# Kernel optimization log

Hardware: AMD Instinct MI355X
Metric: run time of the kernel (lower is better)

The kernel has to match this reference:

```python
import jax, jax.numpy as jnp
import numpy as np

N = 50000   # nodes
E = 400000  # edges
R = 35      # num_relations
B = 12      # num_bases
C = 128     # hidden_conv_dim (heads=1)
T = 4       # node types: load, gen, load_gen, ext
HL = 38     # hidden_lin_dim
OUT = 2


def setup_inputs() -> dict:
    key = jax.random.key(0)
    ks = jax.random.split(key, 24)
    s = 0.1  # param scale
    inp = {
        'x': jax.random.normal(ks[0], (N, 2), jnp.float32),
        'edge_index': jax.random.randint(ks[1], (2, E), 0, N, jnp.int32),
        'edge_type': jax.random.randint(ks[2], (E,), 0, R, jnp.int32),
        'edge_attr': jax.random.normal(ks[3], (E, 2), jnp.float32),
        'node_type': jax.random.randint(ks[4], (N,), 0, T, jnp.int32),
        'basis': jax.random.normal(ks[5], (B, 2, C), jnp.float32) * s,
        'att_rel': jax.random.normal(ks[6], (R, B), jnp.float32) * s,
        'q_att': jax.random.normal(ks[7], (C, 1), jnp.float32) * s,
        'k_att': jax.random.normal(ks[8], (C, 1), jnp.float32) * s,
        'e_att': jax.random.normal(ks[9], (C, 1), jnp.float32) * s,
        'lin_edge_W': jax.random.normal(ks[10], (2, C), jnp.float32) * s,
        'conv_bias': jax.random.normal(ks[11], (C,), jnp.float32) * s,
        'lin0_W': jax.random.normal(ks[12], (T, C, HL), jnp.float32) * s,
        'lin0_b': jax.random.normal(ks[13], (T, HL), jnp.float32) * s,
        'lin1_W': jax.random.normal(ks[14], (T, HL, HL), jnp.float32) * s,
        'lin1_b': jax.random.normal(ks[15], (T, HL), jnp.float32) * s,
        'lin2_W': jax.random.normal(ks[16], (T, HL, HL), jnp.float32) * s,
        'lin2_b': jax.random.normal(ks[17], (T, HL), jnp.float32) * s,
        'fin_W': jax.random.normal(ks[18], (T, HL, OUT), jnp.float32) * s,
        'fin_b': jax.random.normal(ks[19], (T, OUT), jnp.float32) * s,
    }
    return inp


def _segment_softmax(alpha, dst, n):
    # PyG softmax: max is detached, eps=1e-16 on the denominator
    amax = jax.lax.stop_gradient(jax.ops.segment_max(alpha, dst, num_segments=n))
    ex = jnp.exp(alpha - amax[dst])
    den = jax.ops.segment_sum(ex, dst, num_segments=n) + 1e-16
    return ex / den[dst]


def _per_type_linear(xv, W, b, t):
    # apply node-type-specific Linear: [N,d] x [T,d,h] -> pick row type
    y = jnp.einsum('nd,tdh->nth', xv, W)              # [N,T,h]
    y = jnp.take_along_axis(y, t[:, None, None], axis=1)[:, 0]
    return y + b[t]


def reference(x, edge_index, edge_type, edge_attr, node_type,
              basis, att_rel, q_att, k_att, e_att, lin_edge_W, conv_bias,
              lin0_W, lin0_b, lin1_W, lin1_b, lin2_W, lin2_b, fin_W, fin_b):
    n = x.shape[0]
    src, dst = edge_index[0], edge_index[1]
    # RGATConv with basis decomposition: per-relation weight [R, in=2, C]
    w = jnp.einsum('rb,bio->rio', att_rel, basis)
    w_e = w[edge_type]                                 # [E,2,C] edge gather
    out_i = jnp.einsum('ei,eic->ec', x[dst], w_e)      # [E,C]
    out_j = jnp.einsum('ei,eic->ec', x[src], w_e)      # [E,C]
    ke = (edge_attr @ lin_edge_W) @ e_att              # [E,1]
    alpha = out_i @ q_att + out_j @ k_att + ke         # additive self-attention
    alpha = jax.nn.leaky_relu(alpha, 0.2)
    alpha = _segment_softmax(alpha, dst, n)            # across-relation segment softmax
    msg = alpha * out_j                                # heads=1 -> [E,C]
    agg = jax.ops.segment_sum(msg, dst, num_segments=n) + conv_bias
    h = jax.nn.leaky_relu(agg, 0.2)                    # forward activation (dropout: eval)
    t = node_type
    h = _per_type_linear(jax.nn.relu(h), lin0_W, lin0_b, t)
    h = _per_type_linear(jax.nn.relu(h), lin1_W, lin1_b, t)
    h = _per_type_linear(jax.nn.relu(h), lin2_W, lin2_b, t)
    out = _per_type_linear(h, fin_W, fin_b, t)         # [N,2]
    # load nodes (type 0): second output passes through abs
    load_out = jnp.concatenate([out[:, :1], jnp.abs(out[:, 1:2])], axis=1)
    return jnp.where((t == 0)[:, None], load_out, out)
```

## Files before the change

kernel.cpp:

```cpp
#include <hip/hip_runtime.h>
#include <math.h>

#define N_NODES 50000
#define N_EDGES 400000
#define R_REL   35
#define B_BASES 12
#define C_DIM   128
#define HL_DIM  38
#define RI2     70
#define NP      50304
#define NB_HIST 196
#define NBUCK   786
#define EPB     2048
#define CAP     704

#define OFF_WT     0
#define OFF_WQ     8960
#define OFF_WK     9030
#define OFF_LE     9100
#define OFF_META   9104
#define OFF_HBLK   9120
#define OFF_PERM   10688
#define OFF_INV    60688
#define OFF_ECUR   110992
#define OFF_EREC   111780
#define OFF_W0P    2325156
#define OFF_W1P    2345636
#define OFF_W2P    2351716

#define ST    0
#define HH    0
#define Y0T   0
#define Y1T   3264
#define Y2T   0
#define SM_DINV 8192
#define SM_FW   8256
#define SM_FB   8332
#define LDS_FLOATS 8334

__global__ __launch_bounds__(256) void k_init(const int* __restrict__ node_type,
                                              const float* __restrict__ basis,
                                              const float* __restrict__ att_rel,
                                              const float* __restrict__ q_att,
                                              const float* __restrict__ k_att,
                                              const float* __restrict__ e_att,
                                              const float* __restrict__ lin_edge_W,
                                              const float* __restrict__ lin0_W,
                                              const float* __restrict__ lin1_W,
                                              const float* __restrict__ lin2_W,
                                              float* __restrict__ ws) {
    int b = blockIdx.x, tid = threadIdx.x;
    if (b < NB_HIST) {
        __shared__ int lh[4];
        if (tid < 4) lh[tid] = 0;
        __syncthreads();
        int i = b * 256 + tid;
        if (i < N_NODES) atomicAdd(&lh[node_type[i]], 1);
        __syncthreads();
        if (tid < 4) ((int*)(ws + OFF_HBLK))[b * 4 + tid] = lh[tid];
    } else if (b < NB_HIST + 35) {
        int idx = (b - NB_HIST) * 256 + tid;
        if (idx < RI2 * C_DIM) {
            int c  = idx & (C_DIM - 1);
            int ri = idx >> 7;
            int r = ri >> 1, ii = ri & 1;
            float acc = 0.f;
            #pragma unroll
            for (int bb = 0; bb < B_BASES; ++bb)
                acc += att_rel[r * B_BASES + bb] * basis[(bb * 2 + ii) * C_DIM + c];
            ws[OFF_WT + idx] = acc;
        }
    } else if (b == NB_HIST + 35) {
        for (int i = tid; i < NBUCK; i += 256) ((int*)(ws + OFF_ECUR))[i] = 0;
    } else if (b < NB_HIST + 36 + 36) {
        int lane = tid & 63, wv = tid >> 6;
        int u = (b - (NB_HIST + 36)) * 4 + wv;
        if (u < 2 * RI2) {
            int ri = (u < RI2) ? u : (u - RI2);
            int r = ri >> 1, ii = ri & 1;
            const float* av = att_rel + r * B_BASES;
            const float* bs = basis + ii * C_DIM;
            float w1 = 0.f, w2 = 0.f;
            #pragma unroll
            for (int bb = 0; bb < B_BASES; ++bb) {
                float a = av[bb];
                w1 += a * bs[bb * 2 * C_DIM + lane];
                w2 += a * bs[bb * 2 * C_DIM + 64 + lane];
            }
            const float* qk = (u < RI2) ? q_att : k_att;
            float s = w1 * qk[lane] + w2 * qk[64 + lane];
            #pragma unroll
            for (int off = 32; off; off >>= 1) s += __shfl_xor(s, off, 64);
            if (lane == 0) ws[((u < RI2) ? OFF_WQ : OFF_WK) + ri] = s;
        } else if (u < 2 * RI2 + 2) {
            int j = u - 2 * RI2;
            const float* er = lin_edge_W + j * C_DIM;
            float s = er[lane] * e_att[lane] + er[64 + lane] * e_att[64 + lane];
            #pragma unroll
            for (int off = 32; off; off >>= 1) s += __shfl_xor(s, off, 64);
            if (lane == 0) ws[OFF_LE + j] = s;
        }
    } else {
        int g = (b - (NB_HIST + 36 + 36)) * 256 + tid;
        for (int idx = g; idx < 4 * C_DIM * HL_DIM; idx += 16 * 256) {
            int tt = idx / (C_DIM * HL_DIM);
            int rem = idx - tt * (C_DIM * HL_DIM);
            int cc = rem / HL_DIM, j = rem - cc * HL_DIM;
            ws[OFF_W0P + tt * (C_DIM * 40) + cc * 40 + j] = lin0_W[idx];
        }
        for (int idx = g; idx < 4 * HL_DIM * HL_DIM; idx += 16 * 256) {
            int tt = idx / (HL_DIM * HL_DIM);
            int rem = idx - tt * (HL_DIM * HL_DIM);
            int cc = rem / HL_DIM, j = rem - cc * HL_DIM;
            ws[OFF_W1P + tt * (HL_DIM * 40) + cc * 40 + j] = lin1_W[idx];
            ws[OFF_W2P + tt * (HL_DIM * 40) + cc * 40 + j] = lin2_W[idx];
        }
    }
}

__global__ __launch_bounds__(256) void k_perm(const int* __restrict__ node_type,
                                              float* __restrict__ ws) {
    __shared__ int lh[NB_HIST * 4];
    __shared__ int pre[4], tot[4], basel[4];
    __shared__ int wcnt[4][4];
    int tid = threadIdx.x;
    int lane = tid & 63, wv = tid >> 6;
    const int* hblk = (const int*)(ws + OFF_HBLK);
    for (int i = tid; i < NB_HIST * 4; i += 256) lh[i] = hblk[i];
    __syncthreads();
    if (tid < 4) {
        int run = 0, mypre = 0;
        for (int bb = 0; bb < NB_HIST; ++bb) {
            if (bb == (int)blockIdx.x) mypre = run;
            run += lh[bb * 4 + tid];
        }
        pre[tid] = mypre;
        tot[tid] = run;
    }
    __syncthreads();
    if (tid == 0) {
        int t0 = tot[0], t1 = tot[1], t2 = tot[2];
        int b1 = ((t0 + 63) >> 6) << 6;
        int b2 = b1 + (((t1 + 63) >> 6) << 6);
        int b3 = b2 + (((t2 + 63) >> 6) << 6);
        basel[0] = 0; basel[1] = b1; basel[2] = b2; basel[3] = b3;
        if (blockIdx.x == 0) {
            int* meta = (int*)(ws + OFF_META);
            meta[0] = t0; meta[1] = t1; meta[2] = t2; meta[3] = tot[3];
            meta[4] = 0;  meta[5] = b1; meta[6] = b2; meta[7] = b3;
        }
    }
    __syncthreads();
    int n = blockIdx.x * 256 + tid;
    bool active = n < N_NODES;
    int ty = active ? node_type[n] : -1;
    int myrank = 0;
    #pragma unroll
    for (int t = 0; t < 4; ++t) {
        unsigned long long m = __ballot(ty == t);
        if (lane == 0) wcnt[wv][t] = __popcll(m);
        if (ty == t) myrank = __popcll(m & ((1ULL << lane) - 1ULL));
    }
    __syncthreads();
    if (active) {
        int prew = 0;
        for (int w2 = 0; w2 < wv; ++w2) prew += wcnt[w2][ty];
        int p = basel[ty] + pre[ty] + prew + myrank;
        ((int*)(ws + OFF_PERM))[n] = p;
        ((int*)(ws + OFF_INV))[p] = n;
    }
}

__global__ __launch_bounds__(256) void k_escatter(const float* __restrict__ x,
                                                  const int* __restrict__ edge_index,
                                                  const int* __restrict__ edge_type,
                                                  const float* __restrict__ edge_attr,
                                                  float* __restrict__ ws) {
    __shared__ int hist[NBUCK];
    __shared__ int sbase[NBUCK];
    __shared__ float swq[RI2], swk[RI2], sle[2];
    int tid = threadIdx.x;
    for (int i = tid; i < NBUCK; i += 256) hist[i] = 0;
    if (tid < RI2) { swq[tid] = ws[OFF_WQ + tid]; swk[tid] = ws[OFF_WK + tid]; }
    if (tid < 2) sle[tid] = ws[OFF_LE + tid];
    __syncthreads();

    const int* perm = (const int*)(ws + OFF_PERM);
    int base = blockIdx.x * EPB;
    int   rb[8], rm[8];
    float rex[8], rsx[8], rsy[8];
    #pragma unroll
    for (int k = 0; k < 8; ++k) {
        int e = base + k * 256 + tid;
        rb[k] = -1;
        if (e < N_EDGES) {
            int src = edge_index[e];
            int dst = edge_index[N_EDGES + e];
            int r   = edge_type[e];
            int p   = perm[dst];
            float2 ea = *(const float2*)(edge_attr + 2 * e);
            float2 xs = *(const float2*)(x + 2 * src);
            float2 xd = *(const float2*)(x + 2 * dst);
            float alpha = xd.x * swq[2 * r] + xd.y * swq[2 * r + 1]
                        + xs.x * swk[2 * r] + xs.y * swk[2 * r + 1]
                        + ea.x * sle[0]     + ea.y * sle[1];
            alpha = alpha > 0.f ? alpha : 0.2f * alpha;
            float ex = __expf(alpha);
            rb[k]  = p >> 6;
            rm[k]  = (r << 6) | (p & 63);
            rex[k] = ex;
            rsx[k] = ex * xs.x;
            rsy[k] = ex * xs.y;
            atomicAdd(&hist[rb[k]], 1);
        }
    }
    __syncthreads();
    int* gcur = (int*)(ws + OFF_ECUR);
    for (int i = tid; i < NBUCK; i += 256) {
        int c = hist[i];
        sbase[i] = (c > 0) ? atomicAdd(&gcur[i], c) : 0;
    }
    __syncthreads();
    float4* rec = (float4*)(ws + OFF_EREC);
    #pragma unroll
    for (int k = 0; k < 8; ++k) {
        if (rb[k] >= 0) {
            int slot = atomicAdd(&sbase[rb[k]], 1);
            rec[(size_t)rb[k] * CAP + slot] =
                make_float4(__int_as_float(rm[k]), rex[k], rsx[k], rsy[k]);
        }
    }
}

__global__ __launch_bounds__(256, 4) void k_node(
        const float* __restrict__ ws, const float* __restrict__ conv_bias,
        const float* __restrict__ lin0_b, const float* __restrict__ lin1_b,
        const float* __restrict__ lin2_b, const float* __restrict__ fin_W,
        const float* __restrict__ fin_b, float* __restrict__ out) {
    __shared__ float L[LDS_FLOATS];
    int tid  = threadIdx.x;
    int lane = tid & 63;
    int wv   = tid >> 6;
    int p0   = blockIdx.x * 64;

    const int* meta = (const int*)(ws + OFF_META);
    int b1 = meta[5], b2 = meta[6], b3 = meta[7];
    int t  = (p0 >= b1) + (p0 >= b2) + (p0 >= b3);
    int bp = meta[4 + t];
    int cnt = meta[t];

    for (int i4 = tid; i4 < (RI2 * 68) / 4; i4 += 256)
        *(float4*)&L[ST + i4 * 4] = make_float4(0.f, 0.f, 0.f, 0.f);
    if (tid < 64) L[SM_DINV + tid] = 0.f;
    if (tid >= 64 && tid < 142) {
        int i = tid - 64;
        if (i < 76) L[SM_FW + i] = fin_W[t * 76 + i];
        else        L[SM_FB + i - 76] = fin_b[t * 2 + i - 76];
    }
    __syncthreads();

    {
        int ecnt = ((const int*)(ws + OFF_ECUR))[blockIdx.x];
        const float4* rec = (const float4*)(ws + OFF_EREC) + (size_t)blockIdx.x * CAP;
        for (int i = tid; i < ecnt; i += 256) {
            float4 v = rec[i];
            int m = __float_as_int(v.x);
            int n = m & 63, r = m >> 6;
            atomicAdd(&L[ST + (2 * r) * 68 + n],     v.z);
            atomicAdd(&L[ST + (2 * r + 1) * 68 + n], v.w);
            atomicAdd(&L[SM_DINV + n],               v.y);
        }
    }
    __syncthreads();
    if (tid < 64) L[SM_DINV + tid] = 1.0f / (L[SM_DINV + tid] + 1e-16f);

    int ng = lane & 15, cg_ = lane >> 4;
    int c0 = wv * 32 + cg_ * 8;
    const float* wTg = ws + OFF_WT;
    float acc[32];
    #pragma unroll
    for (int i = 0; i < 32; ++i) acc[i] = 0.f;
    #pragma unroll 5
    for (int kk = 0; kk < RI2; ++kk) {
        float4 a4 = *(const float4*)&L[ST + kk * 68 + ng * 4];
        float4 wa = *(const float4*)&wTg[kk * 128 + c0];
        float4 wc = *(const float4*)&wTg[kk * 128 + c0 + 4];
        float a_[4] = {a4.x, a4.y, a4.z, a4.w};
        float w_[8] = {wa.x, wa.y, wa.z, wa.w, wc.x, wc.y, wc.z, wc.w};
        #pragma unroll
        for (int ni = 0; ni < 4; ++ni)
            #pragma unroll
            for (int ci = 0; ci < 8; ++ci)
                acc[ni * 8 + ci] += a_[ni] * w_[ci];
    }
    __syncthreads();

    {
        float4 dv = *(const float4*)&L[SM_DINV + ng * 4];
        float d_[4] = {dv.x, dv.y, dv.z, dv.w};
        #pragma unroll
        for (int ci = 0; ci < 8; ++ci) {
            float cb = conv_bias[c0 + ci];
            float4 hv;
            float h0 = acc[0 * 8 + ci] * d_[0] + cb;
            float h1 = acc[1 * 8 + ci] * d_[1] + cb;
            float h2 = acc[2 * 8 + ci] * d_[2] + cb;
            float h3 = acc[3 * 8 + ci] * d_[3] + cb;
            hv.x = h0 > 0.f ? h0 : 0.f;
            hv.y = h1 > 0.f ? h1 : 0.f;
            hv.z = h2 > 0.f ? h2 : 0.f;
            hv.w = h3 > 0.f ? h3 : 0.f;
            *(float4*)&L[HH + (c0 + ci) * 64 + ng * 4] = hv;
        }
    }
    __syncthreads();

    int jg = lane >> 4;
    int j0 = wv * 16 + jg * 4;
    const float* W0g = ws + OFF_W0P + t * (C_DIM * 40);
    float acc2[16];
    #pragma unroll
    for (int i = 0; i < 16; ++i) acc2[i] = 0.f;
    if (wv < 3) {
        #pragma unroll 4
        for (int kk = 0; kk < C_DIM; ++kk) {
            float4 a4 = *(const float4*)&L[HH + kk * 64 + ng * 4];
            float4 w4 = *(const float4*)&W0g[kk * 40 + j0];
            float a_[4] = {a4.x, a4.y, a4.z, a4.w};
            float w_[4] = {w4.x, w4.y, w4.z, w4.w};
            #pragma unroll
            for (int ni = 0; ni < 4; ++ni)
                #pragma unroll
                for (int ji = 0; ji < 4; ++ji)
                    acc2[ni * 4 + ji] += a_[ni] * w_[ji];
        }
    }
    __syncthreads();

    if (wv < 3) {
        #pragma unroll
        for (int ji = 0; ji < 4; ++ji) {
            int j = j0 + ji;
            float b = (j < HL_DIM) ? lin0_b[t * HL_DIM + j] : 0.f;
            float4 yv;
            float y0 = acc2[0 * 4 + ji] + b;
            float y1 = acc2[1 * 4 + ji] + b;
            float y2 = acc2[2 * 4 + ji] + b;
            float y3 = acc2[3 * 4 + ji] + b;
            yv.x = y0 > 0.f ? y0 : 0.f;
            yv.y = y1 > 0.f ? y1 : 0.f;
            yv.z = y2 > 0.f ? y2 : 0.f;
            yv.w = y3 > 0.f ? y3 : 0.f;
            *(float4*)&L[Y0T + j * 68 + ng * 4] = yv;
        }
    }
    __syncthreads();

    if (wv < 3) {
        const float* W1g = ws + OFF_W1P + t * (HL_DIM * 40);
        float acc3[16];
        #pragma unroll
        for (int i = 0; i < 16; ++i) acc3[i] = 0.f;
        #pragma unroll 2
        for (int kk = 0; kk < HL_DIM; ++kk) {
            float4 a4 = *(const float4*)&L[Y0T + kk * 68 + ng * 4];
            float4 w4 = *(const float4*)&W1g[kk * 40 + j0];
            float a_[4] = {a4.x, a4.y, a4.z, a4.w};
            float w_[4] = {w4.x, w4.y, w4.z, w4.w};
            #pragma unroll
            for (int ni = 0; ni < 4; ++ni)
                #pragma unroll
                for (int ji = 0; ji < 4; ++ji)
                    acc3[ni * 4 + ji] += a_[ni] * w_[ji];
        }
        #pragma unroll
        for (int ji = 0; ji < 4; ++ji) {
            int j = j0 + ji;
            float b = (j < HL_DIM) ? lin1_b[t * HL_DIM + j] : 0.f;
            float4 yv;
            float y0 = acc3[0 * 4 + ji] + b;
            float y1 = acc3[1 * 4 + ji] + b;
            float y2 = acc3[2 * 4 + ji] + b;
            float y3 = acc3[3 * 4 + ji] + b;
            yv.x = y0 > 0.f ? y0 : 0.f;
            yv.y = y1 > 0.f ? y1 : 0.f;
            yv.z = y2 > 0.f ? y2 : 0.f;
            yv.w = y3 > 0.f ? y3 : 0.f;
            *(float4*)&L[Y1T + j * 68 + ng * 4] = yv;
        }
    }
    __syncthreads();

    if (wv < 3) {
        const float* W2g = ws + OFF_W2P + t * (HL_DIM * 40);
        float acc4[16];
        #pragma unroll
        for (int i = 0; i < 16; ++i) acc4[i] = 0.f;
        #pragma unroll 2
        for (int kk = 0; kk < HL_DIM; ++kk) {
            float4 a4 = *(const float4*)&L[Y1T + kk * 68 + ng * 4];
            float4 w4 = *(const float4*)&W2g[kk * 40 + j0];
            float a_[4] = {a4.x, a4.y, a4.z, a4.w};
            float w_[4] = {w4.x, w4.y, w4.z, w4.w};
            #pragma unroll
            for (int ni = 0; ni < 4; ++ni)
                #pragma unroll
                for (int ji = 0; ji < 4; ++ji)
                    acc4[ni * 4 + ji] += a_[ni] * w_[ji];
        }
        #pragma unroll
        for (int ji = 0; ji < 4; ++ji) {
            int j = j0 + ji;
            float b = (j < HL_DIM) ? lin2_b[t * HL_DIM + j] : 0.f;
            float4 yv;
            yv.x = acc4[0 * 4 + ji] + b;
            yv.y = acc4[1 * 4 + ji] + b;
            yv.z = acc4[2 * 4 + ji] + b;
            yv.w = acc4[3 * 4 + ji] + b;
            *(float4*)&L[Y2T + j * 68 + ng * 4] = yv;
        }
    }
    __syncthreads();

    if (tid < 64) {
        int p = p0 + tid;
        bool valid = (p - bp) < cnt;
        float o0 = L[SM_FB], o1 = L[SM_FB + 1];
        for (int jj = 0; jj < HL_DIM; ++jj) {
            float v = L[Y2T + jj * 68 + tid];
            float2 f = *(const float2*)&L[SM_FW + jj * 2];
            o0 += v * f.x;
            o1 += v * f.y;
        }
        if (t == 0) o1 = fabsf(o1);
        if (valid) {
            int orig = ((const int*)(ws + OFF_INV))[p];
            ((float2*)out)[orig] = make_float2(o0, o1);
        }
    }
}

extern "C" void kernel_launch(void* const* d_in, const int* in_sizes, int n_in,
                              void* d_out, int out_size, void* d_ws, size_t ws_size,
                              hipStream_t stream) {
    const float* x          = (const float*)d_in[0];
    const int*   edge_index = (const int*)  d_in[1];
    const int*   edge_type  = (const int*)  d_in[2];
    const float* edge_attr  = (const float*)d_in[3];
    const int*   node_type  = (const int*)  d_in[4];
    const float* basis      = (const float*)d_in[5];
    const float* att_rel    = (const float*)d_in[6];
    const float* q_att      = (const float*)d_in[7];
    const float* k_att      = (const float*)d_in[8];
    const float* e_att      = (const float*)d_in[9];
    const float* lin_edge_W = (const float*)d_in[10];
    const float* conv_bias  = (const float*)d_in[11];
    const float* lin0_W     = (const float*)d_in[12];
    const float* lin0_b     = (const float*)d_in[13];
    const float* lin1_W     = (const float*)d_in[14];
    const float* lin1_b     = (const float*)d_in[15];
    const float* lin2_W     = (const float*)d_in[16];
    const float* lin2_b     = (const float*)d_in[17];
    const float* fin_W      = (const float*)d_in[18];
    const float* fin_b      = (const float*)d_in[19];

    float* ws  = (float*)d_ws;
    float* out = (float*)d_out;

    k_init    <<<NB_HIST + 35 + 1 + 36 + 16, 256, 0, stream>>>(node_type, basis, att_rel,
                                                               q_att, k_att, e_att, lin_edge_W,
                                                               lin0_W, lin1_W, lin2_W, ws);
    k_perm    <<<NB_HIST, 256, 0, stream>>>(node_type, ws);
    k_escatter<<<NB_HIST, 256, 0, stream>>>(x, edge_index, edge_type, edge_attr, ws);
    k_node    <<<NBUCK, 256, 0, stream>>>(ws, conv_bias,
                                          lin0_b, lin1_b, lin2_b, fin_W, fin_b, out);
}
```

Baseline: 168.6 us.

## Merge init and perm kernels; fold weight prep into edge scatter

Cuts the launch chain from four kernels to three. The type histogram and block prefix are now computed redundantly in every block of the new k_prep kernel, which rescans all node types, instead of a separate histogram pass. The basis-combine and weight-packing work moves into extra blocks of k_escatter. The q/k attention scalars are recomputed per block via an algebraic refactoring: basis·q dot products first, then combined with att_rel. The cost is that each of the 196 blocks rereads the 50000 node types, plus some redundant per-block prep.

Result: slower. 203.0 us (+20.4%).

```diff
diff --git a/kernel.cpp b/kernel.cpp
--- a/kernel.cpp
+++ b/kernel.cpp
@@ -15,11 +15,7 @@
 #define CAP     704
 
 #define OFF_WT     0
-#define OFF_WQ     8960
-#define OFF_WK     9030
-#define OFF_LE     9100
 #define OFF_META   9104
-#define OFF_HBLK   9120
 #define OFF_PERM   10688
 #define OFF_INV    60688
 #define OFF_ECUR   110992
@@ -38,120 +34,56 @@
 #define SM_FB   8332
 #define LDS_FLOATS 8334
 
-__global__ __launch_bounds__(256) void k_init(const int* __restrict__ node_type,
-                                              const float* __restrict__ basis,
-                                              const float* __restrict__ att_rel,
-                                              const float* __restrict__ q_att,
-                                              const float* __restrict__ k_att,
-                                              const float* __restrict__ e_att,
-                                              const float* __restrict__ lin_edge_W,
-                                              const float* __restrict__ lin0_W,
-                                              const float* __restrict__ lin1_W,
-                                              const float* __restrict__ lin2_W,
+__global__ __launch_bounds__(256) void k_prep(const int* __restrict__ node_type,
                                               float* __restrict__ ws) {
     int b = blockIdx.x, tid = threadIdx.x;
-    if (b < NB_HIST) {
-        __shared__ int lh[4];
-        if (tid < 4) lh[tid] = 0;
-        __syncthreads();
-        int i = b * 256 + tid;
-        if (i < N_NODES) atomicAdd(&lh[node_type[i]], 1);
-        __syncthreads();
-        if (tid < 4) ((int*)(ws + OFF_HBLK))[b * 4 + tid] = lh[tid];
-    } else if (b < NB_HIST + 35) {
-        int idx = (b - NB_HIST) * 256 + tid;
-        if (idx < RI2 * C_DIM) {
-            int c  = idx & (C_DIM - 1);
-            int ri = idx >> 7;
-            int r = ri >> 1, ii = ri & 1;
-            float acc = 0.f;
-            #pragma unroll
-            for (int bb = 0; bb < B_BASES; ++bb)
-                acc += att_rel[r * B_BASES + bb] * basis[(bb * 2 + ii) * C_DIM + c];
-            ws[OFF_WT + idx] = acc;
-        }
-    } else if (b == NB_HIST + 35) {
+    if (b >= NB_HIST) {
         for (int i = tid; i < NBUCK; i += 256) ((int*)(ws + OFF_ECUR))[i] = 0;
-    } else if (b < NB_HIST + 36 + 36) {
-        int lane = tid & 63, wv = tid >> 6;
-        int u = (b - (NB_HIST + 36)) * 4 + wv;
-        if (u < 2 * RI2) {
-            int ri = (u < RI2) ? u : (u - RI2);
-            int r = ri >> 1, ii = ri & 1;
-            const float* av = att_rel + r * B_BASES;
-            const float* bs = basis + ii * C_DIM;
-            float w1 = 0.f, w2 = 0.f;
-            #pragma unroll
-            for (int bb = 0; bb < B_BASES; ++bb) {
-                float a = av[bb];
-                w1 += a * bs[bb * 2 * C_DIM + lane];
-                w2 += a * bs[bb * 2 * C_DIM + 64 + lane];
-            }
-            const float* qk = (u < RI2) ? q_att : k_att;
-            float s = w1 * qk[lane] + w2 * qk[64 + lane];
-            #pragma unroll
-            for (int off = 32; off; off >>= 1) s += __shfl_xor(s, off, 64);
-            if (lane == 0) ws[((u < RI2) ? OFF_WQ : OFF_WK) + ri] = s;
-        } else if (u < 2 * RI2 + 2) {
-            int j = u - 2 * RI2;
-            const float* er = lin_edge_W + j * C_DIM;
-            float s = er[lane] * e_att[lane] + er[64 + lane] * e_att[64 + lane];
-            #pragma unroll
-            for (int off = 32; off; off >>= 1) s += __shfl_xor(s, off, 64);
-            if (lane == 0) ws[OFF_LE + j] = s;
-        }
-    } else {
-        int g = (b - (NB_HIST + 36 + 36)) * 256 + tid;
-        for (int idx = g; idx < 4 * C_DIM * HL_DIM; idx += 16 * 256) {
-            int tt = idx / (C_DIM * HL_DIM);
-            int rem = idx - tt * (C_DIM * HL_DIM);
-            int cc = rem / HL_DIM, j = rem - cc * HL_DIM;
-            ws[OFF_W0P + tt * (C_DIM * 40) + cc * 40 + j] = lin0_W[idx];
-        }
-        for (int idx = g; idx < 4 * HL_DIM * HL_DIM; idx += 16 * 256) {
-            int tt = idx / (HL_DIM * HL_DIM);
-            int rem = idx - tt * (HL_DIM * HL_DIM);
-            int cc = rem / HL_DIM, j = rem - cc * HL_DIM;
-            ws[OFF_W1P + tt * (HL_DIM * 40) + cc * 40 + j] = lin1_W[idx];
-            ws[OFF_W2P + tt * (HL_DIM * 40) + cc * 40 + j] = lin2_W[idx];
-        }
-    }
-}
-
-__global__ __launch_bounds__(256) void k_perm(const int* __restrict__ node_type,
-                                              float* __restrict__ ws) {
-    __shared__ int lh[NB_HIST * 4];
-    __shared__ int pre[4], tot[4], basel[4];
+        return;
+    }
+    __shared__ int sred[4][8];
+    __shared__ int fin[8];
+    __shared__ int basel[4];
     __shared__ int wcnt[4][4];
-    int tid = threadIdx.x;
     int lane = tid & 63, wv = tid >> 6;
-    const int* hblk = (const int*)(ws + OFF_HBLK);
-    for (int i = tid; i < NB_HIST * 4; i += 256) lh[i] = hblk[i];
-    __syncthreads();
-    if (tid < 4) {
-        int run = 0, mypre = 0;
-        for (int bb = 0; bb < NB_HIST; ++bb) {
-            if (bb == (int)blockIdx.x) mypre = run;
-            run += lh[bb * 4 + tid];
-        }
-        pre[tid] = mypre;
-        tot[tid] = run;
-    }
+    int limit = b * 256;
+
+    int n0 = 0, n1 = 0, n2 = 0, n3 = 0, q0 = 0, q1 = 0, q2 = 0, q3 = 0;
+    for (int i = tid; i < N_NODES; i += 256) {
+        int ty = node_type[i];
+        int lt = (i < limit) ? 1 : 0;
+        n0 += (ty == 0); n1 += (ty == 1); n2 += (ty == 2); n3 += (ty == 3);
+        q0 += (ty == 0) & lt; q1 += (ty == 1) & lt;
+        q2 += (ty == 2) & lt; q3 += (ty == 3) & lt;
+    }
+    #pragma unroll
+    for (int off = 32; off; off >>= 1) {
+        n0 += __shfl_xor(n0, off, 64); n1 += __shfl_xor(n1, off, 64);
+        n2 += __shfl_xor(n2, off, 64); n3 += __shfl_xor(n3, off, 64);
+        q0 += __shfl_xor(q0, off, 64); q1 += __shfl_xor(q1, off, 64);
+        q2 += __shfl_xor(q2, off, 64); q3 += __shfl_xor(q3, off, 64);
+    }
+    if (lane == 0) {
+        sred[wv][0] = n0; sred[wv][1] = n1; sred[wv][2] = n2; sred[wv][3] = n3;
+        sred[wv][4] = q0; sred[wv][5] = q1; sred[wv][6] = q2; sred[wv][7] = q3;
+    }
+    __syncthreads();
+    if (tid < 8) fin[tid] = sred[0][tid] + sred[1][tid] + sred[2][tid] + sred[3][tid];
     __syncthreads();
     if (tid == 0) {
-        int t0 = tot[0], t1 = tot[1], t2 = tot[2];
+        int t0 = fin[0], t1 = fin[1], t2 = fin[2];
         int b1 = ((t0 + 63) >> 6) << 6;
         int b2 = b1 + (((t1 + 63) >> 6) << 6);
         int b3 = b2 + (((t2 + 63) >> 6) << 6);
         basel[0] = 0; basel[1] = b1; basel[2] = b2; basel[3] = b3;
-        if (blockIdx.x == 0) {
+        if (b == 0) {
             int* meta = (int*)(ws + OFF_META);
-            meta[0] = t0; meta[1] = t1; meta[2] = t2; meta[3] = tot[3];
+            meta[0] = t0; meta[1] = t1; meta[2] = t2; meta[3] = fin[3];
             meta[4] = 0;  meta[5] = b1; meta[6] = b2; meta[7] = b3;
         }
     }
     __syncthreads();
-    int n = blockIdx.x * 256 + tid;
+    int n = b * 256 + tid;
     bool active = n < N_NODES;
     int ty = active ? node_type[n] : -1;
     int myrank = 0;
@@ -165,7 +97,7 @@
     if (active) {
         int prew = 0;
         for (int w2 = 0; w2 < wv; ++w2) prew += wcnt[w2][ty];
-        int p = basel[ty] + pre[ty] + prew + myrank;
+        int p = basel[ty] + fin[4 + ty] + prew + myrank;
         ((int*)(ws + OFF_PERM))[n] = p;
         ((int*)(ws + OFF_INV))[p] = n;
     }
@@ -175,18 +107,87 @@
                                                   const int* __restrict__ edge_index,
                                                   const int* __restrict__ edge_type,
                                                   const float* __restrict__ edge_attr,
+                                                  const float* __restrict__ basis,
+                                                  const float* __restrict__ att_rel,
+                                                  const float* __restrict__ q_att,
+                                                  const float* __restrict__ k_att,
+                                                  const float* __restrict__ e_att,
+                                                  const float* __restrict__ lin_edge_W,
+                                                  const float* __restrict__ lin0_W,
+                                                  const float* __restrict__ lin1_W,
+                                                  const float* __restrict__ lin2_W,
                                                   float* __restrict__ ws) {
+    int b = blockIdx.x, tid = threadIdx.x;
+    if (b >= NB_HIST) {
+        if (b < NB_HIST + 35) {
+            int idx = (b - NB_HIST) * 256 + tid;
+            if (idx < RI2 * C_DIM) {
+                int c  = idx & (C_DIM - 1);
+                int ri = idx >> 7;
+                int r = ri >> 1, ii = ri & 1;
+                float acc = 0.f;
+                #pragma unroll
+                for (int bb = 0; bb < B_BASES; ++bb)
+                    acc += att_rel[r * B_BASES + bb] * basis[(bb * 2 + ii) * C_DIM + c];
+                ws[OFF_WT + idx] = acc;
+            }
+        } else {
+            int g = (b - (NB_HIST + 35)) * 256 + tid;
+            for (int idx = g; idx < 4 * C_DIM * HL_DIM; idx += 16 * 256) {
+                int tt = idx / (C_DIM * HL_DIM);
+                int rem = idx - tt * (C_DIM * HL_DIM);
+                int cc = rem / HL_DIM, j = rem - cc * HL_DIM;
+                ws[OFF_W0P + tt * (C_DIM * 40) + cc * 40 + j] = lin0_W[idx];
+            }
+            for (int idx = g; idx < 4 * HL_DIM * HL_DIM; idx += 16 * 256) {
+                int tt = idx / (HL_DIM * HL_DIM);
+                int rem = idx - tt * (HL_DIM * HL_DIM);
+                int cc = rem / HL_DIM, j = rem - cc * HL_DIM;
+                ws[OFF_W1P + tt * (HL_DIM * 40) + cc * 40 + j] = lin1_W[idx];
+                ws[OFF_W2P + tt * (HL_DIM * 40) + cc * 40 + j] = lin2_W[idx];
+            }
+        }
+        return;
+    }
+
     __shared__ int hist[NBUCK];
     __shared__ int sbase[NBUCK];
     __shared__ float swq[RI2], swk[RI2], sle[2];
-    int tid = threadIdx.x;
+    __shared__ float s_dot[64];
+    int lane = tid & 63, wv = tid >> 6;
+
     for (int i = tid; i < NBUCK; i += 256) hist[i] = 0;
-    if (tid < RI2) { swq[tid] = ws[OFF_WQ + tid]; swk[tid] = ws[OFF_WK + tid]; }
-    if (tid < 2) sle[tid] = ws[OFF_LE + tid];
+
+    for (int task = wv; task < 50; task += 4) {
+        const float* v;
+        const float* o;
+        if (task < 24)      { v = basis + task * C_DIM;           o = q_att; }
+        else if (task < 48) { v = basis + (task - 24) * C_DIM;    o = k_att; }
+        else                { v = lin_edge_W + (task - 48) * C_DIM; o = e_att; }
+        float s = v[lane] * o[lane] + v[64 + lane] * o[64 + lane];
+        #pragma unroll
+        for (int off = 32; off; off >>= 1) s += __shfl_xor(s, off, 64);
+        if (lane == 0) s_dot[task] = s;
+    }
+    __syncthreads();
+    if (tid < RI2) {
+        int r = tid >> 1, ii = tid & 1;
+        float a1 = 0.f, a2 = 0.f;
+        #pragma unroll
+        for (int bb = 0; bb < B_BASES; ++bb) {
+            float a = att_rel[r * B_BASES + bb];
+            a1 += a * s_dot[2 * bb + ii];
+            a2 += a * s_dot[24 + 2 * bb + ii];
+        }
+        swq[tid] = a1;
+        swk[tid] = a2;
+    } else if (tid < RI2 + 2) {
+        sle[tid - RI2] = s_dot[48 + tid - RI2];
+    }
     __syncthreads();
 
     const int* perm = (const int*)(ws + OFF_PERM);
-    int base = blockIdx.x * EPB;
+    int base = b * EPB;
     int   rb[8], rm[8];
     float rex[8], rsx[8], rsy[8];
     #pragma unroll
@@ -341,12 +342,12 @@
         #pragma unroll
         for (int ji = 0; ji < 4; ++ji) {
             int j = j0 + ji;
-            float b = (j < HL_DIM) ? lin0_b[t * HL_DIM + j] : 0.f;
+            float bb = (j < HL_DIM) ? lin0_b[t * HL_DIM + j] : 0.f;
             float4 yv;
-            float y0 = acc2[0 * 4 + ji] + b;
-            float y1 = acc2[1 * 4 + ji] + b;
-            float y2 = acc2[2 * 4 + ji] + b;
-            float y3 = acc2[3 * 4 + ji] + b;
+            float y0 = acc2[0 * 4 + ji] + bb;
+            float y1 = acc2[1 * 4 + ji] + bb;
+            float y2 = acc2[2 * 4 + ji] + bb;
+            float y3 = acc2[3 * 4 + ji] + bb;
             yv.x = y0 > 0.f ? y0 : 0.f;
             yv.y = y1 > 0.f ? y1 : 0.f;
             yv.z = y2 > 0.f ? y2 : 0.f;
@@ -376,12 +377,12 @@
         #pragma unroll
         for (int ji = 0; ji < 4; ++ji) {
             int j = j0 + ji;
-            float b = (j < HL_DIM) ? lin1_b[t * HL_DIM + j] : 0.f;
+            float bb = (j < HL_DIM) ? lin1_b[t * HL_DIM + j] : 0.f;
             float4 yv;
-            float y0 = acc3[0 * 4 + ji] + b;
-            float y1 = acc3[1 * 4 + ji] + b;
-            float y2 = acc3[2 * 4 + ji] + b;
-            float y3 = acc3[3 * 4 + ji] + b;
+            float y0 = acc3[0 * 4 + ji] + bb;
+            float y1 = acc3[1 * 4 + ji] + bb;
+            float y2 = acc3[2 * 4 + ji] + bb;
+            float y3 = acc3[3 * 4 + ji] + bb;
             yv.x = y0 > 0.f ? y0 : 0.f;
             yv.y = y1 > 0.f ? y1 : 0.f;
             yv.z = y2 > 0.f ? y2 : 0.f;
@@ -411,12 +412,12 @@
         #pragma unroll
         for (int ji = 0; ji < 4; ++ji) {
             int j = j0 + ji;
-            float b = (j < HL_DIM) ? lin2_b[t * HL_DIM + j] : 0.f;
+            float bb = (j < HL_DIM) ? lin2_b[t * HL_DIM + j] : 0.f;
             float4 yv;
-            yv.x = acc4[0 * 4 + ji] + b;
-            yv.y = acc4[1 * 4 + ji] + b;
-            yv.z = acc4[2 * 4 + ji] + b;
-            yv.w = acc4[3 * 4 + ji] + b;
+            yv.x = acc4[0 * 4 + ji] + bb;
+            yv.y = acc4[1 * 4 + ji] + bb;
+            yv.z = acc4[2 * 4 + ji] + bb;
+            yv.w = acc4[3 * 4 + ji] + bb;
             *(float4*)&L[Y2T + j * 68 + ng * 4] = yv;
         }
     }
@@ -467,11 +468,10 @@
     float* ws  = (float*)d_ws;
     float* out = (float*)d_out;
 
-    k_init    <<<NB_HIST + 35 + 1 + 36 + 16, 256, 0, stream>>>(node_type, basis, att_rel,
-                                                               q_att, k_att, e_att, lin_edge_W,
-                                                               lin0_W, lin1_W, lin2_W, ws);
-    k_perm    <<<NB_HIST, 256, 0, stream>>>(node_type, ws);
-    k_escatter<<<NB_HIST, 256, 0, stream>>>(x, edge_index, edge_type, edge_attr, ws);
+    k_prep    <<<NB_HIST + 1, 256, 0, stream>>>(node_type, ws);
+    k_escatter<<<NB_HIST + 35 + 16, 256, 0, stream>>>(x, edge_index, edge_type, edge_attr,
+                                                      basis, att_rel, q_att, k_att, e_att,
+                                                      lin_edge_W, lin0_W, lin1_W, lin2_W, ws);
     k_node    <<<NBUCK, 256, 0, stream>>>(ws, conv_bias,
                                           lin0_b, lin1_b, lin2_b, fin_W, fin_b, out);
 }
```
